# Kernel optimization log

Measured on AMD Instinct MI355X. Metric: run time of the kernel, lower is better.

## Reference

```python
import jax, jax.numpy as jnp
import numpy as np

HIDDEN = 1024
ARC = 500
BATCH = 16
SEQ = 512


def setup_inputs() -> dict:
    key = jax.random.key(0)
    ks = jax.random.split(key, 12)
    s_h = 1.0 / np.sqrt(HIDDEN)
    s_a = 1.0 / np.sqrt(ARC)
    return {
        "hidden_states": jax.random.normal(ks[0], (BATCH, SEQ, HIDDEN), dtype=jnp.float32),
        # head MLP: Linear(hidden->arc), ReLU, (Dropout eval=identity), Linear(arc->arc)
        "w1h": jax.random.uniform(ks[1], (ARC, HIDDEN), jnp.float32, -s_h, s_h),
        "b1h": jax.random.uniform(ks[2], (ARC,), jnp.float32, -s_h, s_h),
        "w2h": jax.random.uniform(ks[3], (ARC, ARC), jnp.float32, -s_a, s_a),
        "b2h": jax.random.uniform(ks[4], (ARC,), jnp.float32, -s_a, s_a),
        # dep MLP
        "w1d": jax.random.uniform(ks[5], (ARC, HIDDEN), jnp.float32, -s_h, s_h),
        "b1d": jax.random.uniform(ks[6], (ARC,), jnp.float32, -s_h, s_h),
        "w2d": jax.random.uniform(ks[7], (ARC, ARC), jnp.float32, -s_a, s_a),
        "b2d": jax.random.uniform(ks[8], (ARC,), jnp.float32, -s_a, s_a),
        # nn.Bilinear(arc, arc, 1, bias=True): weight [1, arc, arc], bias [1]
        "Wb": jax.random.uniform(ks[9], (ARC, ARC), jnp.float32, -s_a, s_a),
        "bb": jax.random.uniform(ks[10], (1,), jnp.float32, -s_a, s_a),
    }


def reference(hidden_states, w1h, b1h, w2h, b2h, w1d, b1d, w2d, b2d, Wb, bb):
    # MLPs (dropout is identity at inference)
    head = jnp.maximum(hidden_states @ w1h.T + b1h, 0.0) @ w2h.T + b2h  # [B,S,A]
    dep = jnp.maximum(hidden_states @ w1d.T + b1d, 0.0) @ w2d.T + b2d  # [B,S,A]
    # seq_len <= 512 already; chunked bilinear == two GEMMs:
    # scores[b,i,j] = head[b,i] @ Wb @ dep[b,j] + bb
    headW = head @ Wb  # [B,S,A]
    arc_scores = jnp.einsum("bia,bja->bij", headW, dep) + bb[0]  # [B,S,S]
    return arc_scores
```

## Files before the change

### kernel.cpp

```cpp
#include <hip/hip_runtime.h>
#include <hip/hip_bf16.h>


#define HIDDEN 1024
#define ARC 500
#define AP 512
#define ROWS 8192

typedef __attribute__((ext_vector_type(4))) float f32x4;
typedef __attribute__((ext_vector_type(8))) short short8;

static __device__ __forceinline__ ushort f2bf(float f) {
  union { float f; unsigned u; } v; v.f = f;
  unsigned r = v.u + 0x7fffu + ((v.u >> 16) & 1u);
  return (ushort)(r >> 16);
}

__global__ void k_prep_all(const float* __restrict__ w1h, const float* __restrict__ b1h,
                           const float* __restrict__ w1d, const float* __restrict__ b1d,
                           const float* __restrict__ w2h, const float* __restrict__ b2h,
                           const float* __restrict__ w2d, const float* __restrict__ b2d,
                           const float* __restrict__ Wb, const float4* __restrict__ hs,
                           ushort* __restrict__ W1, ushort* __restrict__ WbT,
                           ushort* __restrict__ w2hT, ushort* __restrict__ W2,
                           float* __restrict__ b1c, ushort* __restrict__ hs_bf) {
  const int bid = blockIdx.x;
  const int tid = threadIdx.x;
  if (bid < 4096) {
    int idx = bid * 256 + tid;
    int n = idx >> 10, k = idx & 1023;
    float v = 0.f;
    if (n < ARC) v = w1h[(size_t)n * HIDDEN + k];
    else if (n >= AP && n < AP + ARC) v = w1d[(size_t)(n - AP) * HIDDEN + k];
    W1[idx] = f2bf(v);
  } else if (bid < 5120) {
    int idx = (bid - 4096) * 256 + tid;
    int a = idx >> 9, j = idx & 511;
    float v = (a < ARC && j < ARC) ? Wb[(size_t)j * ARC + a] : 0.f;
    WbT[idx] = f2bf(v);
  } else if (bid < 6144) {
    int idx = (bid - 5120) * 256 + tid;
    int k = idx >> 9, j = idx & 511;
    float v = 0.f;
    if (j < ARC) {
      if (k < ARC) v = w2h[(size_t)j * ARC + k];
      else if (k == 511) v = b2h[j];
    }
    w2hT[idx] = f2bf(v);
  } else if (bid < 7168) {
    int idx = (bid - 6144) * 256 + tid;
    int n = idx >> 9, k = idx & 511;
    float v = 0.f;
    if (n < ARC) {
      if (k < ARC) v = w2d[(size_t)n * ARC + k];
      else if (k == 511) v = b2d[n];
    }
    W2[idx] = f2bf(v);
  } else if (bid < 7172) {
    int i = (bid - 7168) * 256 + tid;
    float v = 0.f;
    if (i < ARC) v = b1h[i];
    else if (i == 511 || i == 1023) v = 1.f;
    else if (i >= AP && i < AP + ARC) v = b1d[i - AP];
    b1c[i] = v;
  } else {
    const int n4 = ROWS * HIDDEN / 4;
    int i = (bid - 7172) * 256 + tid;
    for (; i < n4; i += 2048 * 256) {
      float4 v = hs[i];
      ushort4 o;
      o.x = f2bf(v.x); o.y = f2bf(v.y); o.z = f2bf(v.z); o.w = f2bf(v.w);
      *(ushort4*)(hs_bf + (size_t)i * 4) = o;
    }
  }
}

template <int BM, int BN>
__device__ __forceinline__ void gemm_body(
    const ushort* __restrict__ A, const ushort* __restrict__ B,
    const float* __restrict__ bias, int bias_mode,
    void* __restrict__ C, int out_bf16, int relu,
    int lda, int ldb, int ldc, int K, int tm, int tn, ushort* lds) {
  constexpr int WR = BM / 2, WCC = BN / 2;
  constexpr int MFR = WR / 16, NFR = WCC / 16;
  constexpr int CA = BM / 64, CB = BN / 64;
  constexpr int LPS = CA + CB;
  constexpr int BUFSZ = (BM + BN) * 32;

  const int t = threadIdx.x;
  const int w = t >> 6;
  const int l = t & 63;
  const int wr = w >> 1, wc = w & 1;

  f32x4 acc[MFR][NFR];
#pragma unroll
  for (int m = 0; m < MFR; ++m)
#pragma unroll
    for (int n = 0; n < NFR; ++n) acc[m][n] = f32x4{0.f, 0.f, 0.f, 0.f};

  const int srow = w * 16 + (l >> 2);
  const int scol = (((l & 3) ^ ((l >> 3) & 3))) * 8;
  const ushort* ag = A + (size_t)(tm + srow) * lda + scol;
  const ushort* bg = B + (size_t)(tn + srow) * ldb + scol;
  const int lofs = w * 512;

  const int fr = l & 15, fh = l >> 4;
  const int swz = (fr >> 1) & 3;
  const int fAo = (wr * WR + fr) * 32 + (fh ^ swz) * 8;
  const int fBo = (wc * WCC + fr) * 32 + (fh ^ swz) * 8;

  auto stage = [&](int kt, ushort* buf) {
#pragma unroll
    for (int c = 0; c < CA; ++c)
      __builtin_amdgcn_global_load_lds(
          (const __attribute__((address_space(1))) void*)(ag + (size_t)c * 64 * lda + kt),
          (__attribute__((address_space(3))) void*)(buf + lofs + c * 2048), 16, 0, 0);
#pragma unroll
    for (int c = 0; c < CB; ++c)
      __builtin_amdgcn_global_load_lds(
          (const __attribute__((address_space(1))) void*)(bg + (size_t)c * 64 * ldb + kt),
          (__attribute__((address_space(3))) void*)(buf + BM * 32 + lofs + c * 2048), 16, 0, 0);
  };
  auto compute = [&](const ushort* buf) {
    short8 af[MFR], bf[NFR];
#pragma unroll
    for (int m = 0; m < MFR; ++m) af[m] = *(const short8*)(buf + fAo + m * 16 * 32);
#pragma unroll
    for (int n = 0; n < NFR; ++n) bf[n] = *(const short8*)(buf + BM * 32 + fBo + n * 16 * 32);
#pragma unroll
    for (int m = 0; m < MFR; ++m)
#pragma unroll
      for (int n = 0; n < NFR; ++n)
        acc[m][n] = __builtin_amdgcn_mfma_f32_16x16x32_bf16(af[m], bf[n], acc[m][n], 0, 0, 0);
  };

  const int nt = K >> 5;
  stage(0, lds);
  stage(32, lds + BUFSZ);
  int cs = 0, ps = 2;
  for (int ti = 0; ti < nt; ++ti) {
    if (ti + 1 < nt) {
      if constexpr (LPS == 2)      asm volatile("s_waitcnt vmcnt(2)" ::: "memory");
      else if constexpr (LPS == 3) asm volatile("s_waitcnt vmcnt(3)" ::: "memory");
      else                         asm volatile("s_waitcnt vmcnt(4)" ::: "memory");
    } else {
      asm volatile("s_waitcnt vmcnt(0)" ::: "memory");
    }
    __builtin_amdgcn_s_barrier();
    __builtin_amdgcn_sched_barrier(0);
    if (ti + 2 < nt) stage((ti + 2) << 5, lds + ps * BUFSZ);
    compute(lds + cs * BUFSZ);
    cs = (cs == 2) ? 0 : cs + 1;
    ps = (ps == 2) ? 0 : ps + 1;
  }

  const int cr = fh * 4;
  const float bscal = (bias_mode == 2) ? bias[0] : 0.f;
#pragma unroll
  for (int m = 0; m < MFR; ++m) {
#pragma unroll
    for (int n = 0; n < NFR; ++n) {
      const int col = tn + wc * WCC + n * 16 + fr;
      const float bv = (bias_mode == 1) ? bias[col] : bscal;
#pragma unroll
      for (int j = 0; j < 4; ++j) {
        const int row = tm + wr * WR + m * 16 + cr + j;
        float v = acc[m][n][j] + bv;
        if (relu) v = fmaxf(v, 0.f);
        if (out_bf16)
          ((ushort*)C)[(size_t)row * ldc + col] = f2bf(v);
        else
          ((float*)C)[(size_t)row * ldc + col] = v;
      }
    }
  }
}

__global__ __launch_bounds__(256)
void k_g1mt(const ushort* __restrict__ hs_bf, const ushort* __restrict__ W1,
            const float* __restrict__ b1c, ushort* __restrict__ t1,
            const ushort* __restrict__ WbT, const ushort* __restrict__ w2hT,
            ushort* __restrict__ MTb) {
  __shared__ ushort lds[3 * (128 + 64) * 32];
  const int flat = blockIdx.y * 8 + blockIdx.x;
  const int f2 = (flat & 7) * 132 + (flat >> 3);
  if (f2 < 1024) {
    const int by = f2 >> 4, bx = f2 & 15;
    gemm_body<128, 64>(hs_bf, W1, b1c, 1, t1, 1, 1,
                       HIDDEN, HIDDEN, 1024, HIDDEN, by * 128, bx * 64, lds);
  } else {
    const int idx = f2 - 1024;
    gemm_body<128, 64>(WbT, w2hT, nullptr, 0, MTb, 1, 0,
                       AP, AP, AP, AP, (idx >> 3) * 128, (idx & 7) * 64, lds);
  }
}

template <int BM, int BN>
__global__ __launch_bounds__(256)
void k_gemm_rt(const ushort* __restrict__ A, const ushort* __restrict__ B,
               const float* __restrict__ bias, int bias_mode,
               void* __restrict__ C, int out_bf16, int relu,
               int lda, int ldb, int ldc, int K,
               long aBS, long bBS, long cBS) {
  __shared__ ushort lds[3 * (BM + BN) * 32];
  const int gx = gridDim.x, gy = gridDim.y;
  const int gxy = gx * gy;
  const int nwg = gxy * gridDim.z;
  const int flat = (blockIdx.z * gy + blockIdx.y) * gx + blockIdx.x;
  const int q = nwg >> 3;
  const int f2 = (flat & 7) * q + (flat >> 3);
  const int bz = f2 / gxy;
  const int rm = f2 - bz * gxy;
  const int by = rm / gx;
  const int bx = rm - by * gx;

  const ushort* Az = A + (size_t)aBS * bz;
  const ushort* Bz = B + (size_t)bBS * bz;
  void* Cz = out_bf16 ? (void*)((ushort*)C + (size_t)cBS * bz)
                      : (void*)((float*)C + (size_t)cBS * bz);
  gemm_body<BM, BN>(Az, Bz, bias, bias_mode, Cz, out_bf16, relu,
                    lda, ldb, ldc, K, by * BM, bx * BN, lds);
}

extern "C" void kernel_launch(void* const* d_in, const int* in_sizes, int n_in,
                              void* d_out, int out_size, void* d_ws, size_t ws_size,
                              hipStream_t stream) {
  const float* hs  = (const float*)d_in[0];
  const float* w1h = (const float*)d_in[1];
  const float* b1h = (const float*)d_in[2];
  const float* w2h = (const float*)d_in[3];
  const float* b2h = (const float*)d_in[4];
  const float* w1d = (const float*)d_in[5];
  const float* b1d = (const float*)d_in[6];
  const float* w2d = (const float*)d_in[7];
  const float* b2d = (const float*)d_in[8];
  const float* Wb  = (const float*)d_in[9];
  const float* bb  = (const float*)d_in[10];

  char* ws = (char*)d_ws;
  ushort* hs_bf = (ushort*)(ws + 0);
  ushort* W1    = (ushort*)(ws + 16777216);
  ushort* WbT   = (ushort*)(ws + 18874368);
  ushort* w2hT  = (ushort*)(ws + 19398656);
  ushort* MT    = (ushort*)(ws + 19922944);
  ushort* W2    = (ushort*)(ws + 20447232);
  ushort* t1    = (ushort*)(ws + 20971520);
  ushort* hw    = (ushort*)(ws + 37748736);
  float*  b1c   = (float*)(ws + 54525952);
  float*  out   = (float*)d_out;

  k_prep_all<<<9220, 256, 0, stream>>>(w1h, b1h, w1d, b1d, w2h, b2h, w2d, b2d,
                                       Wb, (const float4*)hs,
                                       W1, WbT, w2hT, W2, b1c, hs_bf);

  k_g1mt<<<dim3(8, 132), 256, 0, stream>>>(hs_bf, W1, b1c, t1, WbT, w2hT, MT);

  k_gemm_rt<128, 64><<<dim3(8, 64, 2), 256, 0, stream>>>(
      t1, MT, nullptr, 0, hw, 1, 0, 1024, AP, AP, AP,
      AP, (long)AP * AP, (long)ROWS * AP);

  k_gemm_rt<64, 64><<<dim3(8, 8, 16), 256, 0, stream>>>(
      hw, hw + (size_t)ROWS * AP, bb, 2, out, 0, 0, AP, AP, 512, AP,
      (long)512 * AP, (long)512 * AP, (long)512 * 512);
}
```

Baseline: 169.7 us.

## Enlarge GEMM tiles, tile weight transposes through LDS, raise MFMA priority

The first two GEMMs move from 128x64 to 128x128 tiles and the batched score GEMM from 64x64 to 128x64, with grids shrunk to match. The goal is more operand reuse per workgroup and fewer workgroups. The Wb and w2h transposes in the prep kernel now go through a padded 64x64 LDS tile, so the strided global reads become coalesced. s_setprio is raised around the MFMA compute phase to favour math over loads. The larger tiles raise register and LDS use, which can lower occupancy, and the smaller grids may underfill the CUs.

```diff
diff --git a/kernel.cpp b/kernel.cpp
--- a/kernel.cpp
+++ b/kernel.cpp
@@ -24,6 +24,7 @@
                            ushort* __restrict__ W1, ushort* __restrict__ WbT,
                            ushort* __restrict__ w2hT, ushort* __restrict__ W2,
                            float* __restrict__ b1c, ushort* __restrict__ hs_bf) {
+  __shared__ float tlds[64 * 65];
   const int bid = blockIdx.x;
   const int tid = threadIdx.x;
   if (bid < 4096) {
@@ -35,20 +36,6 @@
     W1[idx] = f2bf(v);
   } else if (bid < 5120) {
     int idx = (bid - 4096) * 256 + tid;
-    int a = idx >> 9, j = idx & 511;
-    float v = (a < ARC && j < ARC) ? Wb[(size_t)j * ARC + a] : 0.f;
-    WbT[idx] = f2bf(v);
-  } else if (bid < 6144) {
-    int idx = (bid - 5120) * 256 + tid;
-    int k = idx >> 9, j = idx & 511;
-    float v = 0.f;
-    if (j < ARC) {
-      if (k < ARC) v = w2h[(size_t)j * ARC + k];
-      else if (k == 511) v = b2h[j];
-    }
-    w2hT[idx] = f2bf(v);
-  } else if (bid < 7168) {
-    int idx = (bid - 6144) * 256 + tid;
     int n = idx >> 9, k = idx & 511;
     float v = 0.f;
     if (n < ARC) {
@@ -56,8 +43,45 @@
       else if (k == 511) v = b2d[n];
     }
     W2[idx] = f2bf(v);
-  } else if (bid < 7172) {
-    int i = (bid - 7168) * 256 + tid;
+  } else if (bid < 5184) {
+    const int tile = bid - 5120;
+    const int ta = tile >> 3, tj = tile & 7;
+#pragma unroll
+    for (int i = 0; i < 16; ++i) {
+      int e = i * 256 + tid;
+      int jl = e >> 6, al = e & 63;
+      int j = tj * 64 + jl, a = ta * 64 + al;
+      tlds[jl * 65 + al] = (j < ARC && a < ARC) ? Wb[(size_t)j * ARC + a] : 0.f;
+    }
+    __syncthreads();
+#pragma unroll
+    for (int i = 0; i < 16; ++i) {
+      int e = i * 256 + tid;
+      int al = e >> 6, jl = e & 63;
+      WbT[(size_t)(ta * 64 + al) * AP + tj * 64 + jl] = f2bf(tlds[jl * 65 + al]);
+    }
+  } else if (bid < 5248) {
+    const int tile = bid - 5184;
+    const int tk = tile >> 3, tj = tile & 7;
+#pragma unroll
+    for (int i = 0; i < 16; ++i) {
+      int e = i * 256 + tid;
+      int jl = e >> 6, kl = e & 63;
+      int j = tj * 64 + jl, k = tk * 64 + kl;
+      tlds[jl * 65 + kl] = (j < ARC && k < ARC) ? w2h[(size_t)j * ARC + k] : 0.f;
+    }
+    __syncthreads();
+#pragma unroll
+    for (int i = 0; i < 16; ++i) {
+      int e = i * 256 + tid;
+      int kl = e >> 6, jl = e & 63;
+      int k = tk * 64 + kl, j = tj * 64 + jl;
+      float v = tlds[jl * 65 + kl];
+      if (k == 511) v = (j < ARC) ? b2h[j] : 0.f;
+      w2hT[(size_t)k * AP + j] = f2bf(v);
+    }
+  } else if (bid < 5252) {
+    int i = (bid - 5248) * 256 + tid;
     float v = 0.f;
     if (i < ARC) v = b1h[i];
     else if (i == 511 || i == 1023) v = 1.f;
@@ -65,7 +89,7 @@
     b1c[i] = v;
   } else {
     const int n4 = ROWS * HIDDEN / 4;
-    int i = (bid - 7172) * 256 + tid;
+    int i = (bid - 5252) * 256 + tid;
     for (; i < n4; i += 2048 * 256) {
       float4 v = hs[i];
       ushort4 o;
@@ -149,7 +173,9 @@
     __builtin_amdgcn_s_barrier();
     __builtin_amdgcn_sched_barrier(0);
     if (ti + 2 < nt) stage((ti + 2) << 5, lds + ps * BUFSZ);
+    __builtin_amdgcn_s_setprio(1);
     compute(lds + cs * BUFSZ);
+    __builtin_amdgcn_s_setprio(0);
     cs = (cs == 2) ? 0 : cs + 1;
     ps = (ps == 2) ? 0 : ps + 1;
   }
@@ -181,17 +207,17 @@
             const float* __restrict__ b1c, ushort* __restrict__ t1,
             const ushort* __restrict__ WbT, const ushort* __restrict__ w2hT,
             ushort* __restrict__ MTb) {
-  __shared__ ushort lds[3 * (128 + 64) * 32];
+  __shared__ ushort lds[3 * (128 + 128) * 32];
   const int flat = blockIdx.y * 8 + blockIdx.x;
-  const int f2 = (flat & 7) * 132 + (flat >> 3);
-  if (f2 < 1024) {
-    const int by = f2 >> 4, bx = f2 & 15;
-    gemm_body<128, 64>(hs_bf, W1, b1c, 1, t1, 1, 1,
-                       HIDDEN, HIDDEN, 1024, HIDDEN, by * 128, bx * 64, lds);
+  const int f2 = (flat & 7) * 66 + (flat >> 3);
+  const int by = f2 >> 3, bx = f2 & 7;
+  if (by < 64) {
+    gemm_body<128, 128>(hs_bf, W1, b1c, 1, t1, 1, 1,
+                        HIDDEN, HIDDEN, 1024, HIDDEN, by * 128, bx * 128, lds);
   } else {
-    const int idx = f2 - 1024;
-    gemm_body<128, 64>(WbT, w2hT, nullptr, 0, MTb, 1, 0,
-                       AP, AP, AP, AP, (idx >> 3) * 128, (idx & 7) * 64, lds);
+    const int idx = (by - 64) * 8 + bx;
+    gemm_body<128, 128>(WbT, w2hT, nullptr, 0, MTb, 1, 0,
+                        AP, AP, AP, AP, (idx >> 2) * 128, (idx & 3) * 128, lds);
   }
 }
 
@@ -249,17 +275,17 @@
   float*  b1c   = (float*)(ws + 54525952);
   float*  out   = (float*)d_out;
 
-  k_prep_all<<<9220, 256, 0, stream>>>(w1h, b1h, w1d, b1d, w2h, b2h, w2d, b2d,
+  k_prep_all<<<7300, 256, 0, stream>>>(w1h, b1h, w1d, b1d, w2h, b2h, w2d, b2d,
                                        Wb, (const float4*)hs,
                                        W1, WbT, w2hT, W2, b1c, hs_bf);
 
-  k_g1mt<<<dim3(8, 132), 256, 0, stream>>>(hs_bf, W1, b1c, t1, WbT, w2hT, MT);
-
-  k_gemm_rt<128, 64><<<dim3(8, 64, 2), 256, 0, stream>>>(
+  k_g1mt<<<dim3(8, 66), 256, 0, stream>>>(hs_bf, W1, b1c, t1, WbT, w2hT, MT);
+
+  k_gemm_rt<128, 128><<<dim3(4, 64, 2), 256, 0, stream>>>(
       t1, MT, nullptr, 0, hw, 1, 0, 1024, AP, AP, AP,
       AP, (long)AP * AP, (long)ROWS * AP);
 
-  k_gemm_rt<64, 64><<<dim3(8, 8, 16), 256, 0, stream>>>(
+  k_gemm_rt<128, 64><<<dim3(8, 4, 16), 256, 0, stream>>>(
       hw, hw + (size_t)ROWS * AP, bb, 2, out, 0, 0, AP, AP, 512, AP,
       (long)512 * AP, (long)512 * AP, (long)512 * 512);
 }
```

Result: faster. 163.8 us (-3.5%).
